# Kernel tuning notes

Hardware: AMD Instinct MI355X
Metric: run time of the kernel (lower is better)

The kernel has to match this reference:

```python
import jax, jax.numpy as jnp
import numpy as np

DIM = 1024
NUM_HEADS = 16
REL_DIM = 32
B, N = 8, 512


def setup_inputs() -> dict:
    key = jax.random.key(0)
    ks = jax.random.split(key, 8)
    s = 0.02
    return {
        "x": jax.random.normal(ks[0], (B, N, DIM), dtype=jnp.float32),
        "rel_bias": jax.random.normal(ks[1], (B, N, N, REL_DIM), dtype=jnp.float32),
        # torch nn.Linear convention: weight (out_features, in_features)
        "W_qkv": jax.random.normal(ks[2], (3 * DIM, DIM), dtype=jnp.float32) * s,
        "b_qkv": jax.random.normal(ks[3], (3 * DIM,), dtype=jnp.float32) * s,
        "W_rel": jax.random.normal(ks[4], (NUM_HEADS, REL_DIM), dtype=jnp.float32) * s,
        "b_rel": jax.random.normal(ks[5], (NUM_HEADS,), dtype=jnp.float32) * s,
        "W_out": jax.random.normal(ks[6], (DIM, DIM), dtype=jnp.float32) * s,
        "b_out": jax.random.normal(ks[7], (DIM,), dtype=jnp.float32) * s,
    }


def reference(x, rel_bias, W_qkv, b_qkv, W_rel, b_rel, W_out, b_out):
    Bx, Nx, D = x.shape
    H = NUM_HEADS
    hd = D // H
    # QKV projection: (B,N,3D) -> (B,N,3,H,hd)
    qkv = (x @ W_qkv.T + b_qkv).reshape(Bx, Nx, 3, H, hd)
    q, k, v = qkv[:, :, 0], qkv[:, :, 1], qkv[:, :, 2]
    scale = hd ** -0.5
    attn = jnp.einsum('bnhd,bmhd->bhnm', q, k) * scale
    # per-pair relative bias projected to heads: (B,N,N,H) -> (B,H,N,N)
    rel = (rel_bias @ W_rel.T + b_rel).transpose(0, 3, 1, 2)
    attn = jax.nn.softmax(attn + rel, axis=-1)
    out = jnp.einsum('bhnm,bmhd->bnhd', attn, v).reshape(Bx, Nx, D)
    return out @ W_out.T + b_out
```

## Files before the change

### kernel.cpp

```cpp
#include <hip/hip_runtime.h>

typedef unsigned short u16;
typedef unsigned int u32;
typedef __attribute__((ext_vector_type(8))) __bf16 bf16x8;
typedef __attribute__((ext_vector_type(4))) float f32x4;

union U8 {
  bf16x8 b;
  uint2 u2[2];
  uint4 u4;
  u32 w[4];
  u16 us[8];
};

__device__ __forceinline__ u16 f2bf(float f) {
  u32 x = __float_as_uint(f);
  x += 0x7FFFu + ((x >> 16) & 1u);
  return (u16)(x >> 16);
}
__device__ __forceinline__ float bf2f(u16 u) {
  return __uint_as_float(((u32)u) << 16);
}
__device__ __forceinline__ u32 cvtpk(float lo, float hi) {
  u32 r;
  asm("v_cvt_pk_bf16_f32 %0, %1, %2" : "=v"(r) : "v"(lo), "v"(hi));
  return r;
}

#define GLOAD16(gp, lp)                                                          \
  __builtin_amdgcn_global_load_lds(                                              \
      (const __attribute__((address_space(1))) unsigned int*)(const void*)(gp),  \
      (__attribute__((address_space(3))) unsigned int*)(void*)(lp), 16, 0, 0)

__global__ void k_convert_all(const float* __restrict__ x, const float* __restrict__ wq,
                              const float* __restrict__ wo, u16* __restrict__ xb,
                              u16* __restrict__ wqb, u16* __restrict__ wob) {
  const int NX = 1048576, NQ = 786432, NO = 262144;
  int idx = blockIdx.x * blockDim.x + threadIdx.x;
  int stride = gridDim.x * blockDim.x;
  for (int i = idx; i < NX + NQ + NO; i += stride) {
    const float4* s;
    ushort4* d;
    int k;
    if (i < NX) { s = (const float4*)x; d = (ushort4*)xb; k = i; }
    else if (i < NX + NQ) { s = (const float4*)wq; d = (ushort4*)wqb; k = i - NX; }
    else { s = (const float4*)wo; d = (ushort4*)wob; k = i - NX - NQ; }
    float4 v = s[k];
    ushort4 o;
    o.x = f2bf(v.x); o.y = f2bf(v.y); o.z = f2bf(v.z); o.w = f2bf(v.w);
    d[k] = o;
  }
}

__global__ __launch_bounds__(256) void k_fused_rel_qkv(
    const float* __restrict__ rb, const float* __restrict__ Wr, const float* __restrict__ br,
    u16* __restrict__ relout, const u16* __restrict__ A, const u16* __restrict__ Bm,
    const float* __restrict__ bias, u16* __restrict__ Qo, u16* __restrict__ Ko,
    u16* __restrict__ Vo) {
  __shared__ u16 Al[128 * 64];
  __shared__ u16 Bl[128 * 64];

  const int blk = blockIdx.x;
  const int t = threadIdx.x;
  const int grp = blk / 35, sl = blk % 35;

  if (sl < 3) {
    const int gid = grp * 3 + sl;
    const int bn = gid % 24, bm = gid / 24;
    const int K = 1024;
    const int lane = t & 63, wid = t >> 6;
    const int g = lane >> 4, i16 = lane & 15;
    const int wm = wid >> 1, wn = wid & 1;

    f32x4 zero = {0.f, 0.f, 0.f, 0.f};
    f32x4 acc[4][4];
#pragma unroll
    for (int mi = 0; mi < 4; ++mi)
#pragma unroll
      for (int ni = 0; ni < 4; ++ni) acc[mi][ni] = zero;

    int srow[4], sgc[4];
#pragma unroll
    for (int i = 0; i < 4; ++i) {
      int ch = wid * 256 + i * 64 + lane;
      int r = ch >> 3, cs = ch & 7;
      srow[i] = r;
      sgc[i] = cs ^ (r & 7);
    }

    for (int k0 = 0; k0 < K; k0 += 64) {
      __syncthreads();
#pragma unroll
      for (int i = 0; i < 4; ++i) {
        const u16* ga = A + (size_t)(bm * 128 + srow[i]) * K + k0 + sgc[i] * 8;
        const u16* gb = Bm + (size_t)(bn * 128 + srow[i]) * K + k0 + sgc[i] * 8;
        GLOAD16(ga, Al + (size_t)(wid * 256 + i * 64) * 8);
        GLOAD16(gb, Bl + (size_t)(wid * 256 + i * 64) * 8);
      }
      __syncthreads();

#pragma unroll
      for (int kk = 0; kk < 2; ++kk) {
        U8 af[4], bfr[4];
#pragma unroll
        for (int mi = 0; mi < 4; ++mi) {
          int row = wm * 64 + mi * 16 + i16;
          int ch = (g + 4 * kk) ^ (row & 7);
          af[mi].u4 = *(const uint4*)(Al + row * 64 + ch * 8);
        }
#pragma unroll
        for (int ni = 0; ni < 4; ++ni) {
          int row = wn * 64 + ni * 16 + i16;
          int ch = (g + 4 * kk) ^ (row & 7);
          bfr[ni].u4 = *(const uint4*)(Bl + row * 64 + ch * 8);
        }
#pragma unroll
        for (int mi = 0; mi < 4; ++mi)
#pragma unroll
          for (int ni = 0; ni < 4; ++ni)
            acc[mi][ni] = __builtin_amdgcn_mfma_f32_16x16x32_bf16(af[mi].b, bfr[ni].b,
                                                                  acc[mi][ni], 0, 0, 0);
      }
    }

#pragma unroll
    for (int mi = 0; mi < 4; ++mi) {
#pragma unroll
      for (int ni = 0; ni < 4; ++ni) {
        int col = bn * 128 + wn * 64 + ni * 16 + i16;
        int row0 = bm * 128 + wm * 64 + mi * 16 + 4 * g;
        float bia = bias[col];
        int tt = col >> 10;
        int h = (col >> 6) & 15;
        int d = col & 63;
        int b = row0 >> 9;
        int n0 = row0 & 511;
        if (tt < 2) {
          u16* dst = (tt == 0) ? Qo : Ko;
#pragma unroll
          for (int j = 0; j < 4; ++j)
            dst[((size_t)(b * 16 + h) * 512 + n0 + j) * 64 + d] = f2bf(acc[mi][ni][j] + bia);
        } else {
          uint2 w;
          w.x = cvtpk(acc[mi][ni][0] + bia, acc[mi][ni][1] + bia);
          w.y = cvtpk(acc[mi][ni][2] + bia, acc[mi][ni][3] + bia);
          *(uint2*)(Vo + ((size_t)(b * 16 + h) * 64 + d) * 512 + n0) = w;
        }
      }
    }
  } else {
    const int rid = grp * 32 + (sl - 3);
    const int mt = rid & 7, ntg = (rid >> 3) & 127, b = rid >> 10;
    const int i16 = t & 15, j = (t >> 4) & 3, c = t >> 6;
    const int nt = ntg >> 2, g = ntg & 3;
    const int n = nt * 16 + 4 * g + j;
    const int m = mt * 64 + c * 16 + i16;

    const float4* rp = (const float4*)(rb + ((size_t)(b * 512 + n) * 512 + m) * 32);
    float4 r4[8];
#pragma unroll
    for (int q = 0; q < 8; ++q) r4[q] = rp[q];

    const size_t obase =
        (((size_t)(b * 16) * 32 + nt) * 8 + mt) * 1024 + c * 256 + (g * 16 + i16) * 4 + j;
#pragma unroll
    for (int h = 0; h < 16; ++h) {
      float acc = br[h];
      const float* w = Wr + h * 32;
#pragma unroll
      for (int q = 0; q < 8; ++q) {
        acc += r4[q].x * w[4 * q + 0] + r4[q].y * w[4 * q + 1] +
               r4[q].z * w[4 * q + 2] + r4[q].w * w[4 * q + 3];
      }
      relout[obase + (size_t)h * 262144] = f2bf(acc);
    }
  }
}

__global__ __launch_bounds__(256) void k_gemm_out(const u16* __restrict__ A,
                                                  const u16* __restrict__ Bm,
                                                  const float* __restrict__ bias,
                                                  float* __restrict__ Co) {
  const int K = 1024;
  __shared__ u16 Al[128 * 64];
  __shared__ u16 Bl[128 * 64];
  const int t = threadIdx.x;
  const int lane = t & 63, wid = t >> 6;
  const int g = lane >> 4, i16 = lane & 15;
  const int wm = wid >> 1, wn = wid & 1;
  const int bm = blockIdx.y, bn = blockIdx.x;

  f32x4 zero = {0.f, 0.f, 0.f, 0.f};
  f32x4 acc[4][4];
#pragma unroll
  for (int mi = 0; mi < 4; ++mi)
#pragma unroll
    for (int ni = 0; ni < 4; ++ni) acc[mi][ni] = zero;

  int srow[4], sgc[4];
#pragma unroll
  for (int i = 0; i < 4; ++i) {
    int ch = wid * 256 + i * 64 + lane;
    int r = ch >> 3, cs = ch & 7;
    srow[i] = r;
    sgc[i] = cs ^ (r & 7);
  }

  for (int k0 = 0; k0 < K; k0 += 64) {
    __syncthreads();
#pragma unroll
    for (int i = 0; i < 4; ++i) {
      GLOAD16(A + (size_t)(bm * 128 + srow[i]) * K + k0 + sgc[i] * 8,
              Al + (size_t)(wid * 256 + i * 64) * 8);
      GLOAD16(Bm + (size_t)(bn * 128 + srow[i]) * K + k0 + sgc[i] * 8,
              Bl + (size_t)(wid * 256 + i * 64) * 8);
    }
    __syncthreads();

#pragma unroll
    for (int kk = 0; kk < 2; ++kk) {
      U8 af[4], bfr[4];
#pragma unroll
      for (int mi = 0; mi < 4; ++mi) {
        int row = wm * 64 + mi * 16 + i16;
        int ch = (g + 4 * kk) ^ (row & 7);
        af[mi].u4 = *(const uint4*)(Al + row * 64 + ch * 8);
      }
#pragma unroll
      for (int ni = 0; ni < 4; ++ni) {
        int row = wn * 64 + ni * 16 + i16;
        int ch = (g + 4 * kk) ^ (row & 7);
        bfr[ni].u4 = *(const uint4*)(Bl + row * 64 + ch * 8);
      }
#pragma unroll
      for (int mi = 0; mi < 4; ++mi)
#pragma unroll
        for (int ni = 0; ni < 4; ++ni)
          acc[mi][ni] = __builtin_amdgcn_mfma_f32_16x16x32_bf16(af[mi].b, bfr[ni].b,
                                                                acc[mi][ni], 0, 0, 0);
    }
  }

#pragma unroll
  for (int mi = 0; mi < 4; ++mi) {
#pragma unroll
    for (int ni = 0; ni < 4; ++ni) {
      int col = bn * 128 + wn * 64 + ni * 16 + i16;
      int row0 = bm * 128 + wm * 64 + mi * 16 + 4 * g;
      float bia = bias[col];
#pragma unroll
      for (int j = 0; j < 4; ++j)
        Co[(size_t)(row0 + j) * 1024 + col] = acc[mi][ni][j] + bia;
    }
  }
}

__global__ __launch_bounds__(256) void k_attn(const u16* __restrict__ Q,
                                              const u16* __restrict__ Kb,
                                              const u16* __restrict__ Vtb,
                                              const u16* __restrict__ Rel,
                                              u16* __restrict__ Out) {
  __shared__ u16 Kl[2][64 * 64];
  __shared__ u16 Vl[2][64 * 64];
  __shared__ u16 Pl[4][16 * 68];

  const int qt = blockIdx.x, h = blockIdx.y, b = blockIdx.z;
  const int t = threadIdx.x, lane = t & 63, wid = t >> 6;
  const int g = lane >> 4, i16 = lane & 15;
  const size_t bh = (size_t)(b * 16 + h);

  const u16* Qg = Q + (bh * 512 + qt * 64 + wid * 16 + i16) * 64;
  U8 qf[2];
  qf[0].u4 = *(const uint4*)(Qg + 8 * g);
  qf[1].u4 = *(const uint4*)(Qg + 8 * g + 32);

  float m_run[4], l_run[4];
  f32x4 zero = {0.f, 0.f, 0.f, 0.f};
  f32x4 acc[4];
#pragma unroll
  for (int c = 0; c < 4; ++c) acc[c] = zero;
#pragma unroll
  for (int j = 0; j < 4; ++j) { m_run[j] = -1e30f; l_run[j] = 0.f; }

  int srow[2], sgc[2];
#pragma unroll
  for (int i = 0; i < 2; ++i) {
    int ch = wid * 128 + i * 64 + lane;
    int r = ch >> 3, cs = ch & 7;
    srow[i] = r;
    sgc[i] = cs ^ (r & 7);
  }

  const u16* Kg0 = Kb + bh * 512 * 64;
  const u16* Vg0 = Vtb + bh * 64 * 512;
  const u16* Rg = Rel + ((bh * 32 + qt * 4 + wid) * 8) * 1024 + lane * 4;

#define STAGE(buf, m0)                                                                  \
  do {                                                                                  \
    _Pragma("unroll") for (int i = 0; i < 2; ++i) {                                     \
      GLOAD16(Kg0 + (size_t)((m0) + srow[i]) * 64 + sgc[i] * 8,                         \
              &Kl[buf][(size_t)(wid * 128 + i * 64) * 8]);                              \
      GLOAD16(Vg0 + (size_t)srow[i] * 512 + (m0) + sgc[i] * 8,                          \
              &Vl[buf][(size_t)(wid * 128 + i * 64) * 8]);                              \
    }                                                                                   \
  } while (0)

  STAGE(0, 0);
  __syncthreads();

  for (int it = 0; it < 8; ++it) {
    const int buf = it & 1;
    if (it < 7) STAGE(buf ^ 1, it * 64 + 64);

    uint2 rl[4];
#pragma unroll
    for (int c = 0; c < 4; ++c) rl[c] = *(const uint2*)(Rg + it * 1024 + c * 256);

    f32x4 s[4];
#pragma unroll
    for (int c = 0; c < 4; ++c) s[c] = zero;
    __builtin_amdgcn_s_setprio(1);
#pragma unroll
    for (int c = 0; c < 4; ++c) {
#pragma unroll
      for (int kk = 0; kk < 2; ++kk) {
        int row = c * 16 + i16;
        int ch = (g + 4 * kk) ^ (row & 7);
        U8 kf;
        kf.u4 = *(const uint4*)(&Kl[buf][row * 64 + ch * 8]);
        s[c] = __builtin_amdgcn_mfma_f32_16x16x32_bf16(qf[kk].b, kf.b, s[c], 0, 0, 0);
      }
    }
    __builtin_amdgcn_s_setprio(0);

#pragma unroll
    for (int c = 0; c < 4; ++c) {
      const u16* rc = (const u16*)&rl[c];
#pragma unroll
      for (int j = 0; j < 4; ++j) s[c][j] = s[c][j] * 0.125f + bf2f(rc[j]);
    }
    float fac[4];
#pragma unroll
    for (int j = 0; j < 4; ++j) {
      float pm = fmaxf(fmaxf(s[0][j], s[1][j]), fmaxf(s[2][j], s[3][j]));
      pm = fmaxf(pm, __shfl_xor(pm, 1));
      pm = fmaxf(pm, __shfl_xor(pm, 2));
      pm = fmaxf(pm, __shfl_xor(pm, 4));
      pm = fmaxf(pm, __shfl_xor(pm, 8));
      float mnew = fmaxf(m_run[j], pm);
      fac[j] = __expf(m_run[j] - mnew);
      m_run[j] = mnew;
    }
#pragma unroll
    for (int c = 0; c < 4; ++c)
#pragma unroll
      for (int j = 0; j < 4; ++j) s[c][j] = __expf(s[c][j] - m_run[j]);
#pragma unroll
    for (int j = 0; j < 4; ++j) {
      float rs = s[0][j] + s[1][j] + s[2][j] + s[3][j];
      rs += __shfl_xor(rs, 1);
      rs += __shfl_xor(rs, 2);
      rs += __shfl_xor(rs, 4);
      rs += __shfl_xor(rs, 8);
      l_run[j] = l_run[j] * fac[j] + rs;
    }
#pragma unroll
    for (int c = 0; c < 4; ++c)
#pragma unroll
      for (int j = 0; j < 4; ++j) acc[c][j] *= fac[j];

    u16* Pw = Pl[wid];
#pragma unroll
    for (int c = 0; c < 4; ++c)
#pragma unroll
      for (int j = 0; j < 4; ++j)
        Pw[(4 * g + j) * 68 + c * 16 + i16] = f2bf(s[c][j]);
    __syncthreads();

    U8 pf[2];
#pragma unroll
    for (int kk = 0; kk < 2; ++kk) {
      const u16* p = Pl[wid] + i16 * 68 + 8 * g + 32 * kk;
      pf[kk].u2[0] = *(const uint2*)p;
      pf[kk].u2[1] = *(const uint2*)(p + 4);
    }
    __builtin_amdgcn_s_setprio(1);
#pragma unroll
    for (int c = 0; c < 4; ++c) {
#pragma unroll
      for (int kk = 0; kk < 2; ++kk) {
        int row = c * 16 + i16;
        int ch = (g + 4 * kk) ^ (row & 7);
        U8 vf;
        vf.u4 = *(const uint4*)(&Vl[buf][row * 64 + ch * 8]);
        acc[c] = __builtin_amdgcn_mfma_f32_16x16x32_bf16(pf[kk].b, vf.b, acc[c], 0, 0, 0);
      }
    }
    __builtin_amdgcn_s_setprio(0);
    __syncthreads();
  }
#undef STAGE

#pragma unroll
  for (int c = 0; c < 4; ++c) {
#pragma unroll
    for (int j = 0; j < 4; ++j) {
      int n = qt * 64 + wid * 16 + 4 * g + j;
      float v = acc[c][j] / l_run[j];
      Out[((size_t)b * 512 + n) * 1024 + h * 64 + c * 16 + i16] = f2bf(v);
    }
  }
}

extern "C" void kernel_launch(void* const* d_in, const int* in_sizes, int n_in,
                              void* d_out, int out_size, void* d_ws, size_t ws_size,
                              hipStream_t stream) {
  const float* x = (const float*)d_in[0];
  const float* rel_bias = (const float*)d_in[1];
  const float* W_qkv = (const float*)d_in[2];
  const float* b_qkv = (const float*)d_in[3];
  const float* W_rel = (const float*)d_in[4];
  const float* b_rel = (const float*)d_in[5];
  const float* W_out = (const float*)d_in[6];
  const float* b_out = (const float*)d_in[7];
  float* out = (float*)d_out;

  char* ws = (char*)d_ws;
  u16* x_bf    = (u16*)(ws);
  u16* wqkv_bf = (u16*)(ws + 8388608);
  u16* wout_bf = (u16*)(ws + 14680064);
  u16* Qw      = (u16*)(ws + 16777216);
  u16* Kw      = (u16*)(ws + 25165824);
  u16* Vt      = (u16*)(ws + 33554432);
  u16* relb    = (u16*)(ws + 41943040);
  u16* attno   = (u16*)(ws + 109051904);

  k_convert_all<<<2048, 256, 0, stream>>>(x, W_qkv, W_out, x_bf, wqkv_bf, wout_bf);

  k_fused_rel_qkv<<<8960, 256, 0, stream>>>(rel_bias, W_rel, b_rel, relb, x_bf, wqkv_bf,
                                            b_qkv, Qw, Kw, Vt);

  k_attn<<<dim3(8, 16, 8), 256, 0, stream>>>(Qw, Kw, Vt, relb, attno);

  k_gemm_out<<<dim3(8, 32), 256, 0, stream>>>(attno, wout_bf, b_out, out);
}
```

Measured before the change: 205.3 us.

## Split fused rel/QKV kernel into separate launches and drop a barrier in attention

Splits the previously interleaved relative-bias projection and QKV GEMM kernel into two separate launches, k_rel and k_gemm_qkv, each with its own grid. This undoes the fusion that let the memory-bound rel work overlap with the compute-bound GEMM, and gives up that overlap in exchange for simpler per-block code and less register and LDS pressure in the rel blocks. It also removes a __syncthreads after each wave writes its P tile to LDS in the attention kernel. Since each wave reads back only its own Pl[wid] region, a block-wide barrier may not be needed, but dropping it without any wave-level fence risks a read-after-write ordering problem on LDS.

```diff
diff --git a/kernel.cpp b/kernel.cpp
--- a/kernel.cpp
+++ b/kernel.cpp
@@ -52,127 +52,125 @@
   }
 }
 
-__global__ __launch_bounds__(256) void k_fused_rel_qkv(
-    const float* __restrict__ rb, const float* __restrict__ Wr, const float* __restrict__ br,
-    u16* __restrict__ relout, const u16* __restrict__ A, const u16* __restrict__ Bm,
-    const float* __restrict__ bias, u16* __restrict__ Qo, u16* __restrict__ Ko,
-    u16* __restrict__ Vo) {
+__global__ __launch_bounds__(256) void k_rel(const float* __restrict__ rb,
+                                             const float* __restrict__ Wr,
+                                             const float* __restrict__ br,
+                                             u16* __restrict__ out) {
+  const int t = threadIdx.x;
+  const int i16 = t & 15, j = (t >> 4) & 3, c = t >> 6;
+  const int mt = blockIdx.x, ntg = blockIdx.y, b = blockIdx.z;
+  const int nt = ntg >> 2, g = ntg & 3;
+  const int n = nt * 16 + 4 * g + j;
+  const int m = mt * 64 + c * 16 + i16;
+
+  const float4* rp = (const float4*)(rb + ((size_t)(b * 512 + n) * 512 + m) * 32);
+  float4 r4[8];
+#pragma unroll
+  for (int q = 0; q < 8; ++q) r4[q] = rp[q];
+
+  const size_t obase =
+      (((size_t)(b * 16) * 32 + nt) * 8 + mt) * 1024 + c * 256 + (g * 16 + i16) * 4 + j;
+#pragma unroll
+  for (int h = 0; h < 16; ++h) {
+    float acc = br[h];
+    const float* w = Wr + h * 32;
+#pragma unroll
+    for (int q = 0; q < 8; ++q) {
+      acc += r4[q].x * w[4 * q + 0] + r4[q].y * w[4 * q + 1] +
+             r4[q].z * w[4 * q + 2] + r4[q].w * w[4 * q + 3];
+    }
+    out[obase + (size_t)h * 262144] = f2bf(acc);
+  }
+}
+
+__global__ __launch_bounds__(256) void k_gemm_qkv(const u16* __restrict__ A,
+                                                  const u16* __restrict__ Bm,
+                                                  const float* __restrict__ bias,
+                                                  u16* __restrict__ Qo, u16* __restrict__ Ko,
+                                                  u16* __restrict__ Vo) {
+  const int K = 1024;
   __shared__ u16 Al[128 * 64];
   __shared__ u16 Bl[128 * 64];
-
-  const int blk = blockIdx.x;
   const int t = threadIdx.x;
-  const int grp = blk / 35, sl = blk % 35;
-
-  if (sl < 3) {
-    const int gid = grp * 3 + sl;
-    const int bn = gid % 24, bm = gid / 24;
-    const int K = 1024;
-    const int lane = t & 63, wid = t >> 6;
-    const int g = lane >> 4, i16 = lane & 15;
-    const int wm = wid >> 1, wn = wid & 1;
-
-    f32x4 zero = {0.f, 0.f, 0.f, 0.f};
-    f32x4 acc[4][4];
-#pragma unroll
-    for (int mi = 0; mi < 4; ++mi)
-#pragma unroll
-      for (int ni = 0; ni < 4; ++ni) acc[mi][ni] = zero;
-
-    int srow[4], sgc[4];
+  const int lane = t & 63, wid = t >> 6;
+  const int g = lane >> 4, i16 = lane & 15;
+  const int wm = wid >> 1, wn = wid & 1;
+  const int bm = blockIdx.y, bn = blockIdx.x;
+
+  f32x4 zero = {0.f, 0.f, 0.f, 0.f};
+  f32x4 acc[4][4];
+#pragma unroll
+  for (int mi = 0; mi < 4; ++mi)
+#pragma unroll
+    for (int ni = 0; ni < 4; ++ni) acc[mi][ni] = zero;
+
+  int srow[4], sgc[4];
+#pragma unroll
+  for (int i = 0; i < 4; ++i) {
+    int ch = wid * 256 + i * 64 + lane;
+    int r = ch >> 3, cs = ch & 7;
+    srow[i] = r;
+    sgc[i] = cs ^ (r & 7);
+  }
+
+  for (int k0 = 0; k0 < K; k0 += 64) {
+    __syncthreads();
 #pragma unroll
     for (int i = 0; i < 4; ++i) {
-      int ch = wid * 256 + i * 64 + lane;
-      int r = ch >> 3, cs = ch & 7;
-      srow[i] = r;
-      sgc[i] = cs ^ (r & 7);
-    }
-
-    for (int k0 = 0; k0 < K; k0 += 64) {
-      __syncthreads();
-#pragma unroll
-      for (int i = 0; i < 4; ++i) {
-        const u16* ga = A + (size_t)(bm * 128 + srow[i]) * K + k0 + sgc[i] * 8;
-        const u16* gb = Bm + (size_t)(bn * 128 + srow[i]) * K + k0 + sgc[i] * 8;
-        GLOAD16(ga, Al + (size_t)(wid * 256 + i * 64) * 8);
-        GLOAD16(gb, Bl + (size_t)(wid * 256 + i * 64) * 8);
-      }
-      __syncthreads();
-
-#pragma unroll
-      for (int kk = 0; kk < 2; ++kk) {
-        U8 af[4], bfr[4];
-#pragma unroll
-        for (int mi = 0; mi < 4; ++mi) {
-          int row = wm * 64 + mi * 16 + i16;
-          int ch = (g + 4 * kk) ^ (row & 7);
-          af[mi].u4 = *(const uint4*)(Al + row * 64 + ch * 8);
-        }
-#pragma unroll
-        for (int ni = 0; ni < 4; ++ni) {
-          int row = wn * 64 + ni * 16 + i16;
-          int ch = (g + 4 * kk) ^ (row & 7);
-          bfr[ni].u4 = *(const uint4*)(Bl + row * 64 + ch * 8);
-        }
-#pragma unroll
-        for (int mi = 0; mi < 4; ++mi)
-#pragma unroll
-          for (int ni = 0; ni < 4; ++ni)
-            acc[mi][ni] = __builtin_amdgcn_mfma_f32_16x16x32_bf16(af[mi].b, bfr[ni].b,
-                                                                  acc[mi][ni], 0, 0, 0);
-      }
-    }
-
-#pragma unroll
-    for (int mi = 0; mi < 4; ++mi) {
+      const u16* ga = A + (size_t)(bm * 128 + srow[i]) * K + k0 + sgc[i] * 8;
+      const u16* gb = Bm + (size_t)(bn * 128 + srow[i]) * K + k0 + sgc[i] * 8;
+      GLOAD16(ga, Al + (size_t)(wid * 256 + i * 64) * 8);
+      GLOAD16(gb, Bl + (size_t)(wid * 256 + i * 64) * 8);
+    }
+    __syncthreads();
+
+#pragma unroll
+    for (int kk = 0; kk < 2; ++kk) {
+      U8 af[4], bfr[4];
+#pragma unroll
+      for (int mi = 0; mi < 4; ++mi) {
+        int row = wm * 64 + mi * 16 + i16;
+        int ch = (g + 4 * kk) ^ (row & 7);
+        af[mi].u4 = *(const uint4*)(Al + row * 64 + ch * 8);
+      }
 #pragma unroll
       for (int ni = 0; ni < 4; ++ni) {
-        int col = bn * 128 + wn * 64 + ni * 16 + i16;
-        int row0 = bm * 128 + wm * 64 + mi * 16 + 4 * g;
-        float bia = bias[col];
-        int tt = col >> 10;
-        int h = (col >> 6) & 15;
-        int d = col & 63;
-        int b = row0 >> 9;
-        int n0 = row0 & 511;
-        if (tt < 2) {
-          u16* dst = (tt == 0) ? Qo : Ko;
-#pragma unroll
-          for (int j = 0; j < 4; ++j)
-            dst[((size_t)(b * 16 + h) * 512 + n0 + j) * 64 + d] = f2bf(acc[mi][ni][j] + bia);
-        } else {
-          uint2 w;
-          w.x = cvtpk(acc[mi][ni][0] + bia, acc[mi][ni][1] + bia);
-          w.y = cvtpk(acc[mi][ni][2] + bia, acc[mi][ni][3] + bia);
-          *(uint2*)(Vo + ((size_t)(b * 16 + h) * 64 + d) * 512 + n0) = w;
-        }
-      }
-    }
-  } else {
-    const int rid = grp * 32 + (sl - 3);
-    const int mt = rid & 7, ntg = (rid >> 3) & 127, b = rid >> 10;
-    const int i16 = t & 15, j = (t >> 4) & 3, c = t >> 6;
-    const int nt = ntg >> 2, g = ntg & 3;
-    const int n = nt * 16 + 4 * g + j;
-    const int m = mt * 64 + c * 16 + i16;
-
-    const float4* rp = (const float4*)(rb + ((size_t)(b * 512 + n) * 512 + m) * 32);
-    float4 r4[8];
-#pragma unroll
-    for (int q = 0; q < 8; ++q) r4[q] = rp[q];
-
-    const size_t obase =
-        (((size_t)(b * 16) * 32 + nt) * 8 + mt) * 1024 + c * 256 + (g * 16 + i16) * 4 + j;
-#pragma unroll
-    for (int h = 0; h < 16; ++h) {
-      float acc = br[h];
-      const float* w = Wr + h * 32;
-#pragma unroll
-      for (int q = 0; q < 8; ++q) {
-        acc += r4[q].x * w[4 * q + 0] + r4[q].y * w[4 * q + 1] +
-               r4[q].z * w[4 * q + 2] + r4[q].w * w[4 * q + 3];
-      }
-      relout[obase + (size_t)h * 262144] = f2bf(acc);
+        int row = wn * 64 + ni * 16 + i16;
+        int ch = (g + 4 * kk) ^ (row & 7);
+        bfr[ni].u4 = *(const uint4*)(Bl + row * 64 + ch * 8);
+      }
+#pragma unroll
+      for (int mi = 0; mi < 4; ++mi)
+#pragma unroll
+        for (int ni = 0; ni < 4; ++ni)
+          acc[mi][ni] = __builtin_amdgcn_mfma_f32_16x16x32_bf16(af[mi].b, bfr[ni].b,
+                                                                acc[mi][ni], 0, 0, 0);
+    }
+  }
+
+#pragma unroll
+  for (int mi = 0; mi < 4; ++mi) {
+#pragma unroll
+    for (int ni = 0; ni < 4; ++ni) {
+      int col = bn * 128 + wn * 64 + ni * 16 + i16;
+      int row0 = bm * 128 + wm * 64 + mi * 16 + 4 * g;
+      float bia = bias[col];
+      int tt = col >> 10;
+      int h = (col >> 6) & 15;
+      int d = col & 63;
+      int b = row0 >> 9;
+      int n0 = row0 & 511;
+      if (tt < 2) {
+        u16* dst = (tt == 0) ? Qo : Ko;
+#pragma unroll
+        for (int j = 0; j < 4; ++j)
+          dst[((size_t)(b * 16 + h) * 512 + n0 + j) * 64 + d] = f2bf(acc[mi][ni][j] + bia);
+      } else {
+        uint2 w;
+        w.x = cvtpk(acc[mi][ni][0] + bia, acc[mi][ni][1] + bia);
+        w.y = cvtpk(acc[mi][ni][2] + bia, acc[mi][ni][3] + bia);
+        *(uint2*)(Vo + ((size_t)(b * 16 + h) * 64 + d) * 512 + n0) = w;
+      }
     }
   }
 }
@@ -375,7 +373,6 @@
 #pragma unroll
       for (int j = 0; j < 4; ++j)
         Pw[(4 * g + j) * 68 + c * 16 + i16] = f2bf(s[c][j]);
-    __syncthreads();
 
     U8 pf[2];
 #pragma unroll
@@ -437,8 +434,9 @@
 
   k_convert_all<<<2048, 256, 0, stream>>>(x, W_qkv, W_out, x_bf, wqkv_bf, wout_bf);
 
-  k_fused_rel_qkv<<<8960, 256, 0, stream>>>(rel_bias, W_rel, b_rel, relb, x_bf, wqkv_bf,
-                                            b_qkv, Qw, Kw, Vt);
+  k_rel<<<dim3(8, 128, 8), 256, 0, stream>>>(rel_bias, W_rel, b_rel, relb);
+
+  k_gemm_qkv<<<dim3(24, 32), 256, 0, stream>>>(x_bf, wqkv_bf, b_qkv, Qw, Kw, Vt);
 
   k_attn<<<dim3(8, 16, 8), 256, 0, stream>>>(Qw, Kw, Vt, relb, attno);
 
```

Result: faster. 191.0 us (-7.0%).
